# Optimization experiments

Hardware: AMD Instinct MI355X
Metric: run time of the kernel (lower is better)

## Reference

```python
import jax, jax.numpy as jnp
import numpy as np

N_NODES = 50000
N_EDGES = 800000
FEAT_DIM = 64
NUM_RELS = 8


def setup_inputs() -> dict:
    key = jax.random.key(0)
    k1, k2, k3, k4, k5 = jax.random.split(key, 5)
    features = jax.random.normal(k1, (N_NODES, FEAT_DIM), dtype=jnp.float32)
    # xavier_uniform with relu gain ~= sqrt(2)*sqrt(6/(D+D))
    limit = np.sqrt(2.0) * np.sqrt(6.0 / (FEAT_DIM + FEAT_DIM))
    weight_r = jax.random.uniform(k2, (NUM_RELS, FEAT_DIM, FEAT_DIM), dtype=jnp.float32,
                                  minval=-limit, maxval=limit)
    src = jax.random.randint(k3, (N_EDGES,), 0, N_NODES, dtype=jnp.int64 if jax.config.jax_enable_x64 else jnp.int32)
    dst = jax.random.randint(k4, (N_EDGES,), 0, N_NODES, dtype=src.dtype)
    etype = jax.random.randint(k5, (N_EDGES,), 0, NUM_RELS, dtype=src.dtype)
    return {"features": features, "weight_r": weight_r, "src": src, "dst": dst, "etype": etype}


def reference(features, weight_r, src, dst, etype):
    N, D = features.shape
    c = 0.2
    # in-degree of each destination node (DGL 'deg' node data)
    deg = jax.ops.segment_sum(jnp.ones(dst.shape, dtype=features.dtype), dst, num_segments=N)
    # relation-batched matmul: h @ W_r for every relation, then gather per edge.
    # [R, N, D] = 8*50000*64 floats -- cheap vs. materializing [E, D, D] weights.
    hw = jnp.einsum('nd,rdf->rnf', features, weight_r)
    msg = hw[etype, src] / deg[dst][:, None]          # [E, D]
    M = jax.ops.segment_sum(msg, dst, num_segments=N)  # scatter-sum mailbox reduce
    updated = jax.nn.relu(c * features + (1.0 - c) * M)
    # DGL only applies reduce to nodes that received messages; others keep h.
    return jnp.where((deg > 0)[:, None], updated, features)
```

## Files before the change

kernel.cpp:

```cpp
#include <hip/hip_runtime.h>
#include <hip/hip_bf16.h>

#define N_NODES 50000
#define N_EDGES 800000
#define FEAT 64
#define NRELS 8
#define NPB 32
#define NBUCK 1563
#define NBP 196
#define BCAP 768
#define FB_BLOCKS 782

typedef __attribute__((ext_vector_type(8))) short bf16x8;
typedef __attribute__((ext_vector_type(4))) float f32x4;

static __host__ __device__ inline size_t align256(size_t x) { return (x + 255) & ~(size_t)255; }

__device__ inline unsigned short f2b(float f) {
    unsigned u = __builtin_bit_cast(unsigned, f);
    unsigned r = (u + 0x7fffu + ((u >> 16) & 1u)) >> 16;
    return (unsigned short)r;
}
__device__ inline float b2f(unsigned short u) {
    unsigned v = ((unsigned)u) << 16;
    return __builtin_bit_cast(float, v);
}

__global__ void bfill_kernel(const int* __restrict__ dst, const int* __restrict__ srcv,
                             const int* __restrict__ et, const float* __restrict__ W,
                             const float* __restrict__ feat,
                             int* __restrict__ bcnt, int* __restrict__ tmp,
                             unsigned short* __restrict__ WtT,
                             unsigned short* __restrict__ Fb, int E, int N) {
    const int t = threadIdx.x;

    if (blockIdx.x >= NBP) {
        const int fbb = blockIdx.x - NBP;
        if (fbb < 32) {
            int i4 = fbb * 256 + t;
            float4 v = ((const float4*)W)[i4];
            int bse = i4 * 4;
            int f0 = bse & 63;
            int rd = bse >> 6;
            int d  = rd & 63;
            int r  = rd >> 6;
            unsigned short* w0 = WtT + ((size_t)(r * 64 + f0) * 64 + d);
            w0[0 * 64] = f2b(v.x);
            w0[1 * 64] = f2b(v.y);
            w0[2 * 64] = f2b(v.z);
            w0[3 * 64] = f2b(v.w);
        }
        const int node = fbb * 64 + (t >> 2);
        if (node >= N) return;
        const int seg = t & 3;
        const float4* F4 = (const float4*)feat + (size_t)node * 16 + seg * 4;
        float4 v0 = F4[0], v1 = F4[1], v2 = F4[2], v3 = F4[3];
        bf16x8 b0, b1;
        b0[0] = (short)f2b(v0.x); b0[1] = (short)f2b(v0.y);
        b0[2] = (short)f2b(v0.z); b0[3] = (short)f2b(v0.w);
        b0[4] = (short)f2b(v1.x); b0[5] = (short)f2b(v1.y);
        b0[6] = (short)f2b(v1.z); b0[7] = (short)f2b(v1.w);
        b1[0] = (short)f2b(v2.x); b1[1] = (short)f2b(v2.y);
        b1[2] = (short)f2b(v2.z); b1[3] = (short)f2b(v2.w);
        b1[4] = (short)f2b(v3.x); b1[5] = (short)f2b(v3.y);
        b1[6] = (short)f2b(v3.z); b1[7] = (short)f2b(v3.w);
        *(bf16x8*)(Fb + (size_t)node * 64 + seg * 16)     = b0;
        *(bf16x8*)(Fb + (size_t)node * 64 + seg * 16 + 8) = b1;
        return;
    }

    __shared__ int hist[NBUCK];
    __shared__ int base[NBUCK];
    __shared__ int lcur[NBUCK];
    for (int j = t; j < NBUCK; j += 256) { hist[j] = 0; lcur[j] = 0; }
    __syncthreads();

    const int4* dst4 = (const int4*)dst;
    const int4* src4 = (const int4*)srcv;
    const int4* et4  = (const int4*)et;
    const int n4 = E >> 2;
    int bk[16], pk[16];
#pragma unroll
    for (int k = 0; k < 4; k++) {
        int i4 = blockIdx.x * 1024 + t + k * 256;
        if (i4 < n4) {
            int4 d = dst4[i4];
            int4 s = src4[i4];
            int4 r = et4[i4];
            const int dd[4] = {d.x, d.y, d.z, d.w};
            const int ss[4] = {s.x, s.y, s.z, s.w};
            const int rr[4] = {r.x, r.y, r.z, r.w};
#pragma unroll
            for (int j = 0; j < 4; j++) {
                int idx = k * 4 + j;
                bk[idx] = dd[j] >> 5;
                pk[idx] = (ss[j] & 0xFFFF) | (rr[j] << 16) | ((dd[j] & 31) << 19);
                atomicAdd(&hist[bk[idx]], 1);
            }
        } else {
#pragma unroll
            for (int j = 0; j < 4; j++) bk[k * 4 + j] = -1;
        }
    }
    __syncthreads();
    for (int j = t; j < NBUCK; j += 256)
        if (hist[j] > 0)
            base[j] = j * BCAP + atomicAdd(&bcnt[j], hist[j]);
    __syncthreads();
#pragma unroll
    for (int k = 0; k < 16; k++) {
        if (bk[k] >= 0) {
            int r = atomicAdd(&lcur[bk[k]], 1);
            int pos = base[bk[k]] + r;
            if (pos < (bk[k] + 1) * BCAP)
                tmp[pos] = pk[k];
        }
    }
}

__global__ __launch_bounds__(256, 4) void fuse_kernel(
    const int* __restrict__ bcnt, const int* __restrict__ tmp,
    const unsigned short* __restrict__ Fb,
    const unsigned short* __restrict__ WtT, const float* __restrict__ feat,
    float* __restrict__ out, int N) {
    __shared__ unsigned short Sb[NRELS][NPB][64];
    __shared__ int sedge[BCAP];
    __shared__ int hist[256];
    __shared__ int noff[NPB + 1];
    __shared__ int wsum[4];
    const int t = threadIdx.x;
    const int bkt = blockIdx.x;
    const int n0 = bkt * NPB;
    const int nn = min(NPB, N - n0);
    const int gid = t >> 3, q = t & 7;

    {
        f32x4 z = {0.f, 0.f, 0.f, 0.f};
        f32x4* zp = (f32x4*)&Sb[0][0][0];
#pragma unroll
        for (int i = 0; i < 8; i++) zp[t + 256 * i] = z;
    }
    hist[t] = 0;
    __syncthreads();

    const int cnt = min(bcnt[bkt], BCAP);
    const int* tb = tmp + (size_t)bkt * BCAP;
    int v0 = (t < cnt) ? tb[t] : -1;
    int v1 = (t + 256 < cnt) ? tb[t + 256] : -1;
    int v2 = (t + 512 < cnt) ? tb[t + 512] : -1;
    if (v0 >= 0) atomicAdd(&hist[(v0 >> 16) & 255], 1);
    if (v1 >= 0) atomicAdd(&hist[(v1 >> 16) & 255], 1);
    if (v2 >= 0) atomicAdd(&hist[(v2 >> 16) & 255], 1);
    __syncthreads();
    const int myc = hist[t];
    int x = myc;
#pragma unroll
    for (int o = 1; o < 64; o <<= 1) {
        int u_ = __shfl_up(x, o);
        if ((t & 63) >= o) x += u_;
    }
    if ((t & 63) == 63) wsum[t >> 6] = x;
    __syncthreads();
    {
        int add = 0;
        const int wv = t >> 6;
        if (wv > 0) add += wsum[0];
        if (wv > 1) add += wsum[1];
        if (wv > 2) add += wsum[2];
        x += add;
    }
    const int ex = x - myc;
    if ((t & 7) == 0) noff[t >> 3] = ex;
    if (t == 255) noff[NPB] = ex + myc;
    hist[t] = ex;
    __syncthreads();
    if (v0 >= 0) { int p = atomicAdd(&hist[(v0 >> 16) & 255], 1); sedge[p] = v0; }
    if (v1 >= 0) { int p = atomicAdd(&hist[(v1 >> 16) & 255], 1); sedge[p] = v1; }
    if (v2 >= 0) { int p = atomicAdd(&hist[(v2 >> 16) & 255], 1); sedge[p] = v2; }
    __syncthreads();

    int b = 0, e = 0;
    if (gid < nn) { b = noff[gid]; e = noff[gid + 1]; }
    if (gid < nn && b < e) {
        const int swz = (q ^ (gid & 7)) * 8;
        unsigned short* srow = &Sb[0][0][0] + (size_t)gid * 64 + swz;
        float a[8] = {0.f, 0.f, 0.f, 0.f, 0.f, 0.f, 0.f, 0.f};
        int curR = -1;

        auto flushS = [&](int rel) {
            bf16x8 v;
#pragma unroll
            for (int k = 0; k < 8; k++) v[k] = (short)f2b(a[k]);
            *(bf16x8*)(srow + (size_t)rel * (NPB * 64)) = v;
        };
        auto issue = [&](int cb, int (&pk)[4], bf16x8 (&u)[4]) {
#pragma unroll
            for (int j = 0; j < 4; j++) {
                int p = (cb + j < e) ? sedge[cb + j] : -1;
                pk[j] = p;
                if (p >= 0)
                    u[j] = *(const bf16x8*)(Fb + (size_t)(p & 0xFFFF) * 64 + q * 8);
            }
        };
        auto consume = [&](int (&pk)[4], bf16x8 (&u)[4]) {
#pragma unroll
            for (int j = 0; j < 4; j++) {
                int p = pk[j];
                if (p >= 0) {
                    bf16x8 uu = u[j];
                    int rel = (p >> 16) & 7;
                    if (rel != curR) {
                        if (curR >= 0) flushS(curR);
                        curR = rel;
#pragma unroll
                        for (int k = 0; k < 8; k++) a[k] = b2f((unsigned short)uu[k]);
                    } else {
#pragma unroll
                        for (int k = 0; k < 8; k++) a[k] += b2f((unsigned short)uu[k]);
                    }
                }
            }
        };

        bf16x8 z8 = {0, 0, 0, 0, 0, 0, 0, 0};
        int pkA[4] = {-1, -1, -1, -1}, pkB[4] = {-1, -1, -1, -1};
        bf16x8 uA[4] = {z8, z8, z8, z8}, uB[4] = {z8, z8, z8, z8};

        issue(b, pkA, uA);
        __builtin_amdgcn_sched_barrier(0);
#pragma unroll
        for (int c = 0; c < 8; c++) {
            const int nb = b + (c + 1) * 4;
            if ((c & 1) == 0) {
                if (c < 7 && nb < e) issue(nb, pkB, uB);
                __builtin_amdgcn_sched_barrier(0);
                consume(pkA, uA);
            } else {
                if (c < 7 && nb < e) issue(nb, pkA, uA);
                __builtin_amdgcn_sched_barrier(0);
                consume(pkB, uB);
            }
            if (nb >= e) break;
        }
        for (int i = b + 32; i < e; i++) {
            int p = sedge[i];
            bf16x8 uu = *(const bf16x8*)(Fb + (size_t)(p & 0xFFFF) * 64 + q * 8);
            int rel = (p >> 16) & 7;
            if (rel != curR) {
                if (curR >= 0) flushS(curR);
                curR = rel;
#pragma unroll
                for (int k = 0; k < 8; k++) a[k] = b2f((unsigned short)uu[k]);
            } else {
#pragma unroll
                for (int k = 0; k < 8; k++) a[k] += b2f((unsigned short)uu[k]);
            }
        }
        if (curR >= 0) flushS(curR);
    }

    float4 h0e = make_float4(0.f, 0.f, 0.f, 0.f), h1e = h0e;
    const int ef0 = q * 8;
    if (gid < nn) {
        const float4* fp = (const float4*)feat + (size_t)(n0 + gid) * 16 + (ef0 >> 2);
        h0e = fp[0];
        h1e = fp[1];
    }
    __syncthreads();

    const int w = t >> 6, l = t & 63, col = l & 15, quad = l >> 4;
    f32x4 acc0 = {0.f, 0.f, 0.f, 0.f}, acc1 = {0.f, 0.f, 0.f, 0.f};
    const int sw0 = (quad ^ (col & 7)) * 8;
    const int sw1 = ((quad + 4) ^ (col & 7)) * 8;
#pragma unroll
    for (int r = 0; r < NRELS; r++) {
        const unsigned short* wp = WtT + (size_t)r * 4096 + ((w * 16 + col) * 64 + quad * 8);
        bf16x8 b0 = *(const bf16x8*)wp;
        bf16x8 b1 = *(const bf16x8*)(wp + 32);
        const unsigned short* Sr = &Sb[0][0][0] + (size_t)r * (NPB * 64);
        bf16x8 a0 = *(const bf16x8*)&Sr[col * 64 + sw0];
        bf16x8 a1 = *(const bf16x8*)&Sr[col * 64 + sw1];
        bf16x8 c0 = *(const bf16x8*)&Sr[(16 + col) * 64 + sw0];
        bf16x8 c1 = *(const bf16x8*)&Sr[(16 + col) * 64 + sw1];
        acc0 = __builtin_amdgcn_mfma_f32_16x16x32_bf16(a0, b0, acc0, 0, 0, 0);
        acc0 = __builtin_amdgcn_mfma_f32_16x16x32_bf16(a1, b1, acc0, 0, 0, 0);
        acc1 = __builtin_amdgcn_mfma_f32_16x16x32_bf16(c0, b0, acc1, 0, 0, 0);
        acc1 = __builtin_amdgcn_mfma_f32_16x16x32_bf16(c1, b1, acc1, 0, 0, 0);
    }
    __syncthreads();

    float* C = (float*)&Sb[0][0][0];
#pragma unroll
    for (int i = 0; i < 4; i++) {
        C[(quad * 4 + i) * 72 + w * 16 + col]        = acc0[i];
        C[(16 + quad * 4 + i) * 72 + w * 16 + col]   = acc1[i];
    }
    __syncthreads();

    if (gid < nn) {
        const int gn = n0 + gid;
        const int deg = e - b;
        float4 m0 = *(const float4*)&C[gid * 72 + ef0];
        float4 m1 = *(const float4*)&C[gid * 72 + ef0 + 4];
        float4 r0, r1;
        if (deg > 0) {
            float inv = 0.8f / (float)deg;
            r0.x = fmaxf(0.2f * h0e.x + m0.x * inv, 0.f);
            r0.y = fmaxf(0.2f * h0e.y + m0.y * inv, 0.f);
            r0.z = fmaxf(0.2f * h0e.z + m0.z * inv, 0.f);
            r0.w = fmaxf(0.2f * h0e.w + m0.w * inv, 0.f);
            r1.x = fmaxf(0.2f * h1e.x + m1.x * inv, 0.f);
            r1.y = fmaxf(0.2f * h1e.y + m1.y * inv, 0.f);
            r1.z = fmaxf(0.2f * h1e.z + m1.z * inv, 0.f);
            r1.w = fmaxf(0.2f * h1e.w + m1.w * inv, 0.f);
        } else {
            r0 = h0e; r1 = h1e;
        }
        float4* op = (float4*)out + (size_t)gn * 16 + (ef0 >> 2);
        op[0] = r0;
        op[1] = r1;
    }
}

__global__ void degf_kernel(const int* __restrict__ dst, float* __restrict__ deg, int E) {
    int e = blockIdx.x * blockDim.x + threadIdx.x;
    if (e < E) atomicAdd(deg + dst[e], 1.0f);
}

__global__ void otf_kernel(const int* __restrict__ src, const int* __restrict__ dst,
                           const int* __restrict__ et, const float* __restrict__ feat,
                           const float* __restrict__ W, float* __restrict__ out, int E) {
    int wid = (blockIdx.x * blockDim.x + threadIdx.x) >> 6;
    int l = threadIdx.x & 63;
    if (wid >= E) return;
    int s = src[wid], dd = dst[wid], r = et[wid];
    float fv = feat[(size_t)s * 64 + l];
    const float* Wr = W + (size_t)r * 4096;
    float acc = 0.f;
#pragma unroll
    for (int d = 0; d < 64; d++) {
        float a = __shfl(fv, d);
        acc += a * Wr[d * 64 + l];
    }
    atomicAdd(out + (size_t)dd * 64 + l, acc);
}

__global__ void final_kernel(const float* __restrict__ feat, const float* __restrict__ deg,
                             float* __restrict__ out, int N) {
    int i = blockIdx.x * blockDim.x + threadIdx.x;
    if (i >= N * 16) return;
    int n = i >> 4;
    float d = deg[n];
    float4 f = ((const float4*)feat)[i];
    float4 m = ((float4*)out)[i];
    float4 res;
    if (d > 0.f) {
        float inv = 0.8f / d;
        res.x = fmaxf(0.2f * f.x + m.x * inv, 0.f);
        res.y = fmaxf(0.2f * f.y + m.y * inv, 0.f);
        res.z = fmaxf(0.2f * f.z + m.z * inv, 0.f);
        res.w = fmaxf(0.2f * f.w + m.w * inv, 0.f);
    } else {
        res = f;
    }
    ((float4*)out)[i] = res;
}

extern "C" void kernel_launch(void* const* d_in, const int* in_sizes, int n_in,
                              void* d_out, int out_size, void* d_ws, size_t ws_size,
                              hipStream_t stream) {
    const float* feat = (const float*)d_in[0];
    const float* W    = (const float*)d_in[1];
    const int*   src  = (const int*)d_in[2];
    const int*   dst  = (const int*)d_in[3];
    const int*   et   = (const int*)d_in[4];
    float* out = (float*)d_out;

    const int N = N_NODES, E = N_EDGES;

    char* p = (char*)d_ws;
    int* bcnt  = (int*)p;  p += align256((size_t)NBUCK * 4);
    int* tmp   = (int*)p;  p += align256((size_t)NBUCK * BCAP * 4);
    unsigned short* WtT = (unsigned short*)p;
    p += align256((size_t)NRELS * FEAT * FEAT * 2);
    unsigned short* Fb = (unsigned short*)p;
    p += align256((size_t)N * FEAT * 2);
    size_t need_full = (size_t)(p - (char*)d_ws);

    if (ws_size >= need_full) {
        hipMemsetAsync(bcnt, 0, (size_t)NBUCK * 4, stream);
        bfill_kernel<<<NBP + FB_BLOCKS, 256, 0, stream>>>(dst, src, et, W, feat,
                                                          bcnt, tmp, WtT, Fb, E, N);
        fuse_kernel<<<NBUCK, 256, 0, stream>>>(bcnt, tmp, Fb, WtT, feat, out, N);
    } else {
        float* deg = (float*)d_ws;
        hipMemsetAsync(out, 0, (size_t)N * FEAT * 4, stream);
        hipMemsetAsync(deg, 0, (size_t)N * 4, stream);
        degf_kernel<<<(E + 255) / 256, 256, 0, stream>>>(dst, deg, E);
        otf_kernel<<<(E + 3) / 4, 256, 0, stream>>>(src, dst, et, feat, W, out, E);
        final_kernel<<<(N * 16 + 255) / 256, 256, 0, stream>>>(feat, deg, out, N);
    }
}
```

Measured before the change: 127.5 us.

## Bin edges into coarse 256-node super-buckets with coalesced staged writes

Result: slower. 140.2 us (+9.9%).

```diff
diff --git a/kernel.cpp b/kernel.cpp
--- a/kernel.cpp
+++ b/kernel.cpp
@@ -5,11 +5,13 @@
 #define N_EDGES 800000
 #define FEAT 64
 #define NRELS 8
+#define NSUP 196
+#define SCAP 5120
+#define NBP 196
+#define FB_BLOCKS 782
 #define NPB 32
 #define NBUCK 1563
-#define NBP 196
 #define BCAP 768
-#define FB_BLOCKS 782
 
 typedef __attribute__((ext_vector_type(8))) short bf16x8;
 typedef __attribute__((ext_vector_type(4))) float f32x4;
@@ -69,17 +71,23 @@
         return;
     }
 
-    __shared__ int hist[NBUCK];
-    __shared__ int base[NBUCK];
-    __shared__ int lcur[NBUCK];
-    for (int j = t; j < NBUCK; j += 256) { hist[j] = 0; lcur[j] = 0; }
+    __shared__ int pkL[4096];
+    __shared__ unsigned char supL[4096];
+    __shared__ int hist[NSUP];
+    __shared__ int lbase[NSUP];
+    __shared__ int gbase[NSUP];
+    __shared__ int lcur[NSUP];
+    __shared__ int wsum[4];
+    __shared__ int totS;
+
+    for (int j = t; j < NSUP; j += 256) hist[j] = 0;
     __syncthreads();
 
     const int4* dst4 = (const int4*)dst;
     const int4* src4 = (const int4*)srcv;
     const int4* et4  = (const int4*)et;
     const int n4 = E >> 2;
-    int bk[16], pk[16];
+    int sup[16], pk[16];
 #pragma unroll
     for (int k = 0; k < 4; k++) {
         int i4 = blockIdx.x * 1024 + t + k * 256;
@@ -93,28 +101,59 @@
 #pragma unroll
             for (int j = 0; j < 4; j++) {
                 int idx = k * 4 + j;
-                bk[idx] = dd[j] >> 5;
-                pk[idx] = (ss[j] & 0xFFFF) | (rr[j] << 16) | ((dd[j] & 31) << 19);
-                atomicAdd(&hist[bk[idx]], 1);
+                sup[idx] = dd[j] >> 8;
+                pk[idx] = (ss[j] & 0xFFFF) | (rr[j] << 16) | ((dd[j] & 255) << 19);
+                atomicAdd(&hist[sup[idx]], 1);
             }
         } else {
 #pragma unroll
-            for (int j = 0; j < 4; j++) bk[k * 4 + j] = -1;
-        }
-    }
-    __syncthreads();
-    for (int j = t; j < NBUCK; j += 256)
-        if (hist[j] > 0)
-            base[j] = j * BCAP + atomicAdd(&bcnt[j], hist[j]);
-    __syncthreads();
+            for (int j = 0; j < 4; j++) sup[k * 4 + j] = -1;
+        }
+    }
+    __syncthreads();
+
+    const int myc = (t < NSUP) ? hist[t] : 0;
+    int x = myc;
+#pragma unroll
+    for (int o = 1; o < 64; o <<= 1) {
+        int u_ = __shfl_up(x, o);
+        if ((t & 63) >= o) x += u_;
+    }
+    if ((t & 63) == 63) wsum[t >> 6] = x;
+    __syncthreads();
+    {
+        int add = 0;
+        const int wv = t >> 6;
+        if (wv > 0) add += wsum[0];
+        if (wv > 1) add += wsum[1];
+        if (wv > 2) add += wsum[2];
+        x += add;
+    }
+    const int ex = x - myc;
+    if (t < NSUP) {
+        lbase[t] = ex;
+        lcur[t] = ex;
+        gbase[t] = t * SCAP + ((myc > 0) ? atomicAdd(&bcnt[t], myc) : 0);
+    }
+    if (t == 255) totS = x;
+    __syncthreads();
+
 #pragma unroll
     for (int k = 0; k < 16; k++) {
-        if (bk[k] >= 0) {
-            int r = atomicAdd(&lcur[bk[k]], 1);
-            int pos = base[bk[k]] + r;
-            if (pos < (bk[k] + 1) * BCAP)
-                tmp[pos] = pk[k];
-        }
+        if (sup[k] >= 0) {
+            int p = atomicAdd(&lcur[sup[k]], 1);
+            pkL[p] = pk[k];
+            supL[p] = (unsigned char)sup[k];
+        }
+    }
+    __syncthreads();
+
+    const int total = totS;
+    for (int s0 = t; s0 < total; s0 += 256) {
+        int sp = supL[s0];
+        int pos = gbase[sp] + (s0 - lbase[sp]);
+        if (pos < (sp + 1) * SCAP)
+            tmp[pos] = pkL[s0];
     }
 }
 
@@ -133,6 +172,7 @@
     const int n0 = bkt * NPB;
     const int nn = min(NPB, N - n0);
     const int gid = t >> 3, q = t & 7;
+    const int sup = bkt >> 3, sub = bkt & 7;
 
     {
         f32x4 z = {0.f, 0.f, 0.f, 0.f};
@@ -143,14 +183,13 @@
     hist[t] = 0;
     __syncthreads();
 
-    const int cnt = min(bcnt[bkt], BCAP);
-    const int* tb = tmp + (size_t)bkt * BCAP;
-    int v0 = (t < cnt) ? tb[t] : -1;
-    int v1 = (t + 256 < cnt) ? tb[t + 256] : -1;
-    int v2 = (t + 512 < cnt) ? tb[t + 512] : -1;
-    if (v0 >= 0) atomicAdd(&hist[(v0 >> 16) & 255], 1);
-    if (v1 >= 0) atomicAdd(&hist[(v1 >> 16) & 255], 1);
-    if (v2 >= 0) atomicAdd(&hist[(v2 >> 16) & 255], 1);
+    const int cnt = min(bcnt[sup], SCAP);
+    const int* tb = tmp + (size_t)sup * SCAP;
+    for (int i = t; i < cnt; i += 256) {
+        int v = tb[i];
+        if (((v >> 24) & 7) == sub)
+            atomicAdd(&hist[(((v >> 19) & 31) << 3) | ((v >> 16) & 7)], 1);
+    }
     __syncthreads();
     const int myc = hist[t];
     int x = myc;
@@ -174,13 +213,21 @@
     if (t == 255) noff[NPB] = ex + myc;
     hist[t] = ex;
     __syncthreads();
-    if (v0 >= 0) { int p = atomicAdd(&hist[(v0 >> 16) & 255], 1); sedge[p] = v0; }
-    if (v1 >= 0) { int p = atomicAdd(&hist[(v1 >> 16) & 255], 1); sedge[p] = v1; }
-    if (v2 >= 0) { int p = atomicAdd(&hist[(v2 >> 16) & 255], 1); sedge[p] = v2; }
+    for (int i = t; i < cnt; i += 256) {
+        int v = tb[i];
+        if (((v >> 24) & 7) == sub) {
+            int p = atomicAdd(&hist[(((v >> 19) & 31) << 3) | ((v >> 16) & 7)], 1);
+            if (p < BCAP)
+                sedge[p] = v;
+        }
+    }
     __syncthreads();
 
     int b = 0, e = 0;
-    if (gid < nn) { b = noff[gid]; e = noff[gid + 1]; }
+    if (gid < nn) {
+        b = min(noff[gid], BCAP);
+        e = min(noff[gid + 1], BCAP);
+    }
     if (gid < nn && b < e) {
         const int swz = (q ^ (gid & 7)) * 8;
         unsigned short* srow = &Sb[0][0][0] + (size_t)gid * 64 + swz;
@@ -379,8 +426,8 @@
     const int N = N_NODES, E = N_EDGES;
 
     char* p = (char*)d_ws;
-    int* bcnt  = (int*)p;  p += align256((size_t)NBUCK * 4);
-    int* tmp   = (int*)p;  p += align256((size_t)NBUCK * BCAP * 4);
+    int* bcnt  = (int*)p;  p += align256((size_t)NSUP * 4);
+    int* tmp   = (int*)p;  p += align256((size_t)NSUP * SCAP * 4);
     unsigned short* WtT = (unsigned short*)p;
     p += align256((size_t)NRELS * FEAT * FEAT * 2);
     unsigned short* Fb = (unsigned short*)p;
@@ -388,7 +435,7 @@
     size_t need_full = (size_t)(p - (char*)d_ws);
 
     if (ws_size >= need_full) {
-        hipMemsetAsync(bcnt, 0, (size_t)NBUCK * 4, stream);
+        hipMemsetAsync(bcnt, 0, (size_t)NSUP * 4, stream);
         bfill_kernel<<<NBP + FB_BLOCKS, 256, 0, stream>>>(dst, src, et, W, feat,
                                                           bcnt, tmp, WtT, Fb, E, N);
         fuse_kernel<<<NBUCK, 256, 0, stream>>>(bcnt, tmp, Fb, WtT, feat, out, N);
```
